# Optimization experiments

Hardware: AMD Instinct MI355X
Metric: run time of the kernel (lower is better)

The kernel has to match this reference:

```python
import jax, jax.numpy as jnp
import numpy as np

N_NODES = 100000
N_EDGES = 3200000
IN_CH = 256
OUT_CH = 256


def setup_inputs() -> dict:
    key = jax.random.key(0)
    k1, k2, k3, k4, k5 = jax.random.split(key, 5)
    x = jax.random.normal(k1, (N_NODES, IN_CH), dtype=jnp.float32)
    src = jax.random.randint(k2, (N_EDGES,), 0, N_NODES, dtype=jnp.int64)
    dst = jax.random.randint(k3, (N_EDGES,), 0, N_NODES, dtype=jnp.int64)
    # match torch uniform(in_channels, tensor): U(-1/sqrt(in), 1/sqrt(in))
    bound = 1.0 / np.sqrt(IN_CH)
    weight = jax.random.uniform(k4, (IN_CH, OUT_CH), minval=-bound, maxval=bound, dtype=jnp.float32)
    bias = jax.random.uniform(k5, (OUT_CH,), minval=-bound, maxval=bound, dtype=jnp.float32)
    return {"x": x, "src": src, "dst": dst, "weight": weight, "bias": bias}


def reference(x, src, dst, weight, bias):
    # paramApply: linear transform
    h = jnp.matmul(x, weight) + bias  # [N, out]
    # SpMM: out[dst] += h[src]  (unweighted adjacency, adj @ h)
    agg = jax.ops.segment_sum(h[src], dst, num_segments=N_NODES)  # [N, out]
    # row-degree normalization: adj.sum(-1) clamped at 1
    deg = jax.ops.segment_sum(jnp.ones((src.shape[0],), dtype=h.dtype), dst, num_segments=N_NODES)
    deg = jnp.maximum(deg, 1.0)[:, None]  # [N, 1]
    return agg / deg
```

## Files before the change

### kernel.cpp

```cpp
#include <hip/hip_runtime.h>

#define N_NODES 100000
#define N_EDGES 3200000
#define CH 256

#define NBUCK 256
#define NBUCK_USED 196
#define PBE 4096
#define EPT 16
#define PGRID ((N_EDGES + PBE - 1) / PBE)

#define WS_DEG    0
#define WS_OFF    524288
#define WS_BCNT   1048576
#define WS_BBASE  1049600
#define WS_BCUR   1050624
#define WS_WTB    1056768
#define WS_ESRC   1310720
#define WS_PACKED 14110720
#define WS_XB     14110720
#define WS_NEED_BF16X (WS_XB + (size_t)N_NODES * CH * 2)

typedef __bf16  bf16x8 __attribute__((ext_vector_type(8)));
typedef float   f32x4  __attribute__((ext_vector_type(4)));

__device__ __forceinline__ unsigned short f2bf(float f) {
    union { float f; unsigned u; } c; c.f = f;
    unsigned r = c.u + 0x7FFF + ((c.u >> 16) & 1);
    return (unsigned short)(r >> 16);
}
__device__ __forceinline__ float bf2f(unsigned short b) {
    union { unsigned u; float f; } c; c.u = (unsigned)b << 16;
    return c.f;
}

__global__ __launch_bounds__(256) void hist_k(const int* __restrict__ dst,
                                              int* __restrict__ bucket_cnt) {
    __shared__ int h[NBUCK];
    int t = threadIdx.x;
    h[t] = 0;
    __syncthreads();
    long e0 = (long)blockIdx.x * PBE;
#pragma unroll
    for (int i = 0; i < EPT; ++i) {
        long e = e0 + i * 256 + t;
        if (e < N_EDGES) atomicAdd(&h[dst[e] >> 9], 1);
    }
    __syncthreads();
    if (h[t]) atomicAdd(&bucket_cnt[t], h[t]);
}

__global__ void bscan_k(const int* __restrict__ cnt, int* __restrict__ base,
                        int* __restrict__ cursor) {
    __shared__ int s[NBUCK];
    int t = threadIdx.x;
    int v0 = cnt[t];
    s[t] = v0;
    __syncthreads();
    for (int st = 1; st < 256; st <<= 1) {
        int v = (t >= st) ? s[t - st] : 0;
        __syncthreads();
        s[t] += v;
        __syncthreads();
    }
    int excl = s[t] - v0;
    base[t] = excl;
    cursor[t] = excl;
}

__global__ __launch_bounds__(256) void partition_k(const int* __restrict__ src,
                                                   const int* __restrict__ dst,
                                                   int* __restrict__ bucket_cursor,
                                                   unsigned* __restrict__ packed) {
    __shared__ int hist[NBUCK];
    __shared__ int gbase[NBUCK];
    int t = threadIdx.x;
    hist[t] = 0;
    __syncthreads();
    long e0 = (long)blockIdx.x * PBE;
    int b[EPT], rank[EPT];
    unsigned pk[EPT];
#pragma unroll
    for (int i = 0; i < EPT; ++i) {
        long e = e0 + i * 256 + t;
        if (e < N_EDGES) {
            int d = dst[e];
            int s = src[e];
            b[i] = d >> 9;
            pk[i] = ((unsigned)(d & 511) << 17) | (unsigned)s;
            rank[i] = atomicAdd(&hist[b[i]], 1);
        } else b[i] = -1;
    }
    __syncthreads();
    int cnt = hist[t];
    if (cnt > 0) gbase[t] = atomicAdd(&bucket_cursor[t], cnt);
    __syncthreads();
#pragma unroll
    for (int i = 0; i < EPT; ++i)
        if (b[i] >= 0) packed[gbase[b[i]] + rank[i]] = pk[i];
}

__global__ __launch_bounds__(256) void build_k(const unsigned* __restrict__ packed,
                                               const int* __restrict__ bucket_base,
                                               const int* __restrict__ bucket_cnt,
                                               int* __restrict__ deg, int* __restrict__ off,
                                               int* __restrict__ edge_src) {
    __shared__ int ldeg[512];
    __shared__ int loff[512];
    __shared__ int lcur[512];
    __shared__ int sscan[256];
    int bk = blockIdx.x;
    int t = threadIdx.x;
    ldeg[t] = 0; ldeg[t + 256] = 0;
    __syncthreads();
    int ebase = bucket_base[bk];
    int ecnt  = bucket_cnt[bk];
    const unsigned* pk = packed + ebase;
    for (int i = t; i < ecnt; i += 256) atomicAdd(&ldeg[pk[i] >> 17], 1);
    __syncthreads();
    int a0 = ldeg[2 * t], a1 = ldeg[2 * t + 1];
    sscan[t] = a0 + a1;
    __syncthreads();
    for (int st = 1; st < 256; st <<= 1) {
        int v = (t >= st) ? sscan[t - st] : 0;
        __syncthreads();
        sscan[t] += v;
        __syncthreads();
    }
    int ex = sscan[t] - (a0 + a1);
    loff[2 * t] = ex;      lcur[2 * t] = ex;
    loff[2 * t + 1] = ex + a0;  lcur[2 * t + 1] = ex + a0;
    __syncthreads();
    int n0 = bk * 512;
#pragma unroll
    for (int j = 0; j < 2; ++j) {
        int dlow = t + j * 256;
        int node = n0 + dlow;
        if (node < N_NODES) {
            deg[node] = ldeg[dlow];
            off[node] = ebase + loff[dlow];
        }
    }
    int* es = edge_src + ebase;
    for (int i = t; i < ecnt; i += 256) {
        unsigned p = pk[i];
        int pos = atomicAdd(&lcur[p >> 17], 1);
        es[pos] = (int)(p & 0x1FFFF);
    }
}

__global__ void cast_w_k(const float* __restrict__ W, unsigned short* __restrict__ Wtb) {
    int n = blockIdx.x;
    int k = threadIdx.x;
    Wtb[n * 256 + k] = f2bf(W[k * 256 + n]);
}

__global__ void cast_x_k(const float* __restrict__ x, unsigned short* __restrict__ xb) {
    int i = blockIdx.x * 256 + threadIdx.x;
    float4 v = reinterpret_cast<const float4*>(x)[i];
    ushort4 o;
    o.x = f2bf(v.x); o.y = f2bf(v.y); o.z = f2bf(v.z); o.w = f2bf(v.w);
    reinterpret_cast<ushort4*>(xb)[i] = o;
}

__global__ void aggregate_bf16_k(const unsigned short* __restrict__ xb,
                                 const int* __restrict__ edge_src,
                                 const int* __restrict__ off, const int* __restrict__ deg,
                                 float* __restrict__ m) {
    int wid = threadIdx.x >> 6;
    int lane = threadIdx.x & 63;
    int node = blockIdx.x * 4 + wid;
    int start = off[node];
    int d = deg[node];
    float4 acc[4];
#pragma unroll
    for (int i = 0; i < 4; ++i) acc[i] = make_float4(0.f, 0.f, 0.f, 0.f);
    const unsigned short* xbl = xb + lane * 4;
    int e = 0;
    for (; e + 4 <= d; e += 4) {
        int s[4];
#pragma unroll
        for (int i = 0; i < 4; ++i) s[i] = edge_src[start + e + i];
#pragma unroll
        for (int i = 0; i < 4; ++i) {
            ushort4 v = *reinterpret_cast<const ushort4*>(xbl + (size_t)s[i] * CH);
            acc[i].x += bf2f(v.x); acc[i].y += bf2f(v.y);
            acc[i].z += bf2f(v.z); acc[i].w += bf2f(v.w);
        }
    }
    for (; e < d; ++e) {
        int s0 = edge_src[start + e];
        ushort4 v = *reinterpret_cast<const ushort4*>(xbl + (size_t)s0 * CH);
        acc[0].x += bf2f(v.x); acc[0].y += bf2f(v.y);
        acc[0].z += bf2f(v.z); acc[0].w += bf2f(v.w);
    }
    acc[0].x += acc[1].x + acc[2].x + acc[3].x;
    acc[0].y += acc[1].y + acc[2].y + acc[3].y;
    acc[0].z += acc[1].z + acc[2].z + acc[3].z;
    acc[0].w += acc[1].w + acc[2].w + acc[3].w;
    float inv = 1.0f / (float)(d > 0 ? d : 1);
    acc[0].x *= inv; acc[0].y *= inv; acc[0].z *= inv; acc[0].w *= inv;
    *reinterpret_cast<float4*>(m + (size_t)node * CH + lane * 4) = acc[0];
}

__global__ void aggregate_f32_k(const float* __restrict__ x, const int* __restrict__ edge_src,
                                const int* __restrict__ off, const int* __restrict__ deg,
                                float* __restrict__ m) {
    int wid = threadIdx.x >> 6;
    int lane = threadIdx.x & 63;
    int node = blockIdx.x * 4 + wid;
    int start = off[node];
    int d = deg[node];
    float4 acc0 = make_float4(0.f, 0.f, 0.f, 0.f);
    float4 acc1 = make_float4(0.f, 0.f, 0.f, 0.f);
    const float* xb = x + (size_t)lane * 4;
    int e = 0;
    for (; e + 2 <= d; e += 2) {
        int s0 = edge_src[start + e];
        int s1 = edge_src[start + e + 1];
        const float4 v0 = *reinterpret_cast<const float4*>(xb + (size_t)s0 * CH);
        const float4 v1 = *reinterpret_cast<const float4*>(xb + (size_t)s1 * CH);
        acc0.x += v0.x; acc0.y += v0.y; acc0.z += v0.z; acc0.w += v0.w;
        acc1.x += v1.x; acc1.y += v1.y; acc1.z += v1.z; acc1.w += v1.w;
    }
    if (e < d) {
        int s0 = edge_src[start + e];
        const float4 v0 = *reinterpret_cast<const float4*>(xb + (size_t)s0 * CH);
        acc0.x += v0.x; acc0.y += v0.y; acc0.z += v0.z; acc0.w += v0.w;
    }
    acc0.x += acc1.x; acc0.y += acc1.y; acc0.z += acc1.z; acc0.w += acc1.w;
    float inv = 1.0f / (float)(d > 0 ? d : 1);
    acc0.x *= inv; acc0.y *= inv; acc0.z *= inv; acc0.w *= inv;
    *reinterpret_cast<float4*>(m + (size_t)node * CH + lane * 4) = acc0;
}

__global__ __launch_bounds__(256) void gemm_mfma_k(float* __restrict__ io,
                                                   const unsigned short* __restrict__ Wtb,
                                                   const float* __restrict__ bias,
                                                   const int* __restrict__ deg) {
    __shared__ unsigned short As[64][264];
    int row0 = blockIdx.x * 64;
    int rows = N_NODES - row0;
    if (rows > 64) rows = 64;
    int tid = threadIdx.x;

#pragma unroll
    for (int i = 0; i < 16; ++i) {
        int f = i * 256 + tid;
        int r = f >> 6;
        int c4 = (f & 63) * 4;
        float4 v = make_float4(0.f, 0.f, 0.f, 0.f);
        if (r < rows)
            v = *reinterpret_cast<const float4*>(io + (size_t)(row0 + r) * CH + c4);
        ushort4 o;
        o.x = f2bf(v.x); o.y = f2bf(v.y); o.z = f2bf(v.z); o.w = f2bf(v.w);
        *reinterpret_cast<ushort4*>(&As[r][c4]) = o;
    }
    __syncthreads();

    int wv = tid >> 6;
    int lane = tid & 63;
    int q = lane >> 4;
    int ln = lane & 15;
    int n0 = wv * 64;

    f32x4 acc[4][4];
#pragma unroll
    for (int mt = 0; mt < 4; ++mt)
#pragma unroll
        for (int nt = 0; nt < 4; ++nt)
            acc[mt][nt] = (f32x4){0.f, 0.f, 0.f, 0.f};

#pragma unroll 2
    for (int kc = 0; kc < 8; ++kc) {
        int koff = kc * 32 + q * 8;
        bf16x8 a[4], b[4];
#pragma unroll
        for (int mt = 0; mt < 4; ++mt)
            a[mt] = *reinterpret_cast<const bf16x8*>(&As[mt * 16 + ln][koff]);
#pragma unroll
        for (int nt = 0; nt < 4; ++nt)
            b[nt] = *reinterpret_cast<const bf16x8*>(Wtb + (size_t)(n0 + nt * 16 + ln) * 256 + koff);
#pragma unroll
        for (int mt = 0; mt < 4; ++mt)
#pragma unroll
            for (int nt = 0; nt < 4; ++nt)
                acc[mt][nt] = __builtin_amdgcn_mfma_f32_16x16x32_bf16(a[mt], b[nt], acc[mt][nt], 0, 0, 0);
    }

    float bv[4];
#pragma unroll
    for (int nt = 0; nt < 4; ++nt) bv[nt] = bias[n0 + nt * 16 + ln];

#pragma unroll
    for (int mt = 0; mt < 4; ++mt) {
#pragma unroll
        for (int r = 0; r < 4; ++r) {
            int row = row0 + mt * 16 + q * 4 + r;
            if (row < N_NODES) {
                float bon = (deg[row] > 0) ? 1.f : 0.f;
                float* po = io + (size_t)row * CH + n0 + ln;
#pragma unroll
                for (int nt = 0; nt < 4; ++nt)
                    po[nt * 16] = acc[mt][nt][r] + bv[nt] * bon;
            }
        }
    }
}

extern "C" void kernel_launch(void* const* d_in, const int* in_sizes, int n_in,
                              void* d_out, int out_size, void* d_ws, size_t ws_size,
                              hipStream_t stream) {
    const float* x    = (const float*)d_in[0];
    const int*   src  = (const int*)d_in[1];
    const int*   dst  = (const int*)d_in[2];
    const float* W    = (const float*)d_in[3];
    const float* bias = (const float*)d_in[4];
    float* out = (float*)d_out;

    char* ws = (char*)d_ws;
    int* deg        = (int*)(ws + WS_DEG);
    int* off        = (int*)(ws + WS_OFF);
    int* bcnt       = (int*)(ws + WS_BCNT);
    int* bbase      = (int*)(ws + WS_BBASE);
    int* bcur       = (int*)(ws + WS_BCUR);
    unsigned short* Wtb = (unsigned short*)(ws + WS_WTB);
    int* edge_src   = (int*)(ws + WS_ESRC);
    unsigned* packed = (unsigned*)(ws + WS_PACKED);
    unsigned short* xb = (unsigned short*)(ws + WS_XB);

    bool use_bf16x = ws_size >= WS_NEED_BF16X;

    hipMemsetAsync(bcnt, 0, NBUCK * sizeof(int), stream);

    hist_k<<<PGRID, 256, 0, stream>>>(dst, bcnt);
    bscan_k<<<1, 256, 0, stream>>>(bcnt, bbase, bcur);
    partition_k<<<PGRID, 256, 0, stream>>>(src, dst, bcur, packed);
    build_k<<<NBUCK_USED, 256, 0, stream>>>(packed, bbase, bcnt, deg, off, edge_src);

    cast_w_k<<<256, 256, 0, stream>>>(W, Wtb);

    if (use_bf16x) {
        cast_x_k<<<(N_NODES * CH / 4) / 256, 256, 0, stream>>>(x, xb);
        aggregate_bf16_k<<<N_NODES / 4, 256, 0, stream>>>(xb, edge_src, off, deg, out);
    } else {
        aggregate_f32_k<<<N_NODES / 4, 256, 0, stream>>>(x, edge_src, off, deg, out);
    }

    gemm_mfma_k<<<(N_NODES + 63) / 64, 256, 0, stream>>>(out, Wtb, bias, deg);
}
```

Baseline: 568.6 us.

## Apply linear transform before aggregation and gather bf16 transformed features

Reorders the computation so the MFMA GEMM runs on x first, producing bias-added h stored as bf16, then aggregates h over edges and normalizes into the output. This removes the separate x cast pass and the GEMM's read-modify-write of the full f32 output, cutting global memory traffic. The aggregation loop is also unrolled to 8 gathers in flight and uses readfirstlane for offsets and degree. Rounding h (rather than x) to bf16 slightly changes numerical error characteristics.

```diff
diff --git a/kernel.cpp b/kernel.cpp
--- a/kernel.cpp
+++ b/kernel.cpp
@@ -18,8 +18,8 @@
 #define WS_WTB    1056768
 #define WS_ESRC   1310720
 #define WS_PACKED 14110720
-#define WS_XB     14110720
-#define WS_NEED_BF16X (WS_XB + (size_t)N_NODES * CH * 2)
+#define WS_HB     14110720
+#define WS_NEED_H (WS_HB + (size_t)N_NODES * CH * 2)
 
 typedef __bf16  bf16x8 __attribute__((ext_vector_type(8)));
 typedef float   f32x4  __attribute__((ext_vector_type(4)));
@@ -155,42 +155,122 @@
     Wtb[n * 256 + k] = f2bf(W[k * 256 + n]);
 }
 
-__global__ void cast_x_k(const float* __restrict__ x, unsigned short* __restrict__ xb) {
-    int i = blockIdx.x * 256 + threadIdx.x;
-    float4 v = reinterpret_cast<const float4*>(x)[i];
-    ushort4 o;
-    o.x = f2bf(v.x); o.y = f2bf(v.y); o.z = f2bf(v.z); o.w = f2bf(v.w);
-    reinterpret_cast<ushort4*>(xb)[i] = o;
-}
-
-__global__ void aggregate_bf16_k(const unsigned short* __restrict__ xb,
-                                 const int* __restrict__ edge_src,
-                                 const int* __restrict__ off, const int* __restrict__ deg,
-                                 float* __restrict__ m) {
+__global__ __launch_bounds__(256) void gemm_h_k(const float* __restrict__ x,
+                                                const unsigned short* __restrict__ Wtb,
+                                                const float* __restrict__ bias,
+                                                unsigned short* __restrict__ hb) {
+    __shared__ unsigned short As[64][264];
+    int row0 = blockIdx.x * 64;
+    int rows = N_NODES - row0;
+    if (rows > 64) rows = 64;
+    int tid = threadIdx.x;
+
+#pragma unroll
+    for (int i = 0; i < 16; ++i) {
+        int f = i * 256 + tid;
+        int r = f >> 6;
+        int c4 = (f & 63) * 4;
+        float4 v = make_float4(0.f, 0.f, 0.f, 0.f);
+        if (r < rows)
+            v = *reinterpret_cast<const float4*>(x + (size_t)(row0 + r) * CH + c4);
+        ushort4 o;
+        o.x = f2bf(v.x); o.y = f2bf(v.y); o.z = f2bf(v.z); o.w = f2bf(v.w);
+        *reinterpret_cast<ushort4*>(&As[r][c4]) = o;
+    }
+    __syncthreads();
+
+    int wv = tid >> 6;
+    int lane = tid & 63;
+    int q = lane >> 4;
+    int ln = lane & 15;
+    int n0 = wv * 64;
+
+    f32x4 acc[4][4];
+#pragma unroll
+    for (int mt = 0; mt < 4; ++mt)
+#pragma unroll
+        for (int nt = 0; nt < 4; ++nt)
+            acc[mt][nt] = (f32x4){0.f, 0.f, 0.f, 0.f};
+
+#pragma unroll 2
+    for (int kc = 0; kc < 8; ++kc) {
+        int koff = kc * 32 + q * 8;
+        bf16x8 a[4], b[4];
+#pragma unroll
+        for (int mt = 0; mt < 4; ++mt)
+            a[mt] = *reinterpret_cast<const bf16x8*>(&As[mt * 16 + ln][koff]);
+#pragma unroll
+        for (int nt = 0; nt < 4; ++nt)
+            b[nt] = *reinterpret_cast<const bf16x8*>(Wtb + (size_t)(n0 + nt * 16 + ln) * 256 + koff);
+#pragma unroll
+        for (int mt = 0; mt < 4; ++mt)
+#pragma unroll
+            for (int nt = 0; nt < 4; ++nt)
+                acc[mt][nt] = __builtin_amdgcn_mfma_f32_16x16x32_bf16(a[mt], b[nt], acc[mt][nt], 0, 0, 0);
+    }
+
+    float bv[4];
+#pragma unroll
+    for (int nt = 0; nt < 4; ++nt) bv[nt] = bias[n0 + nt * 16 + ln];
+
+#pragma unroll
+    for (int mt = 0; mt < 4; ++mt) {
+#pragma unroll
+        for (int r = 0; r < 4; ++r) {
+            int row = row0 + mt * 16 + q * 4 + r;
+            if (row < N_NODES) {
+                unsigned short* po = hb + (size_t)row * CH + n0 + ln;
+#pragma unroll
+                for (int nt = 0; nt < 4; ++nt)
+                    po[nt * 16] = f2bf(acc[mt][nt][r] + bv[nt]);
+            }
+        }
+    }
+}
+
+__global__ void aggregate_h_k(const unsigned short* __restrict__ hb,
+                              const int* __restrict__ edge_src,
+                              const int* __restrict__ off, const int* __restrict__ deg,
+                              float* __restrict__ out) {
     int wid = threadIdx.x >> 6;
     int lane = threadIdx.x & 63;
     int node = blockIdx.x * 4 + wid;
-    int start = off[node];
-    int d = deg[node];
+    int start = __builtin_amdgcn_readfirstlane(off[node]);
+    int d     = __builtin_amdgcn_readfirstlane(deg[node]);
     float4 acc[4];
 #pragma unroll
     for (int i = 0; i < 4; ++i) acc[i] = make_float4(0.f, 0.f, 0.f, 0.f);
-    const unsigned short* xbl = xb + lane * 4;
+    const unsigned short* hbl = hb + lane * 4;
+    const int* es = edge_src + start;
     int e = 0;
+    for (; e + 8 <= d; e += 8) {
+        int s[8];
+#pragma unroll
+        for (int i = 0; i < 8; ++i) s[i] = es[e + i];
+        ushort4 v[8];
+#pragma unroll
+        for (int i = 0; i < 8; ++i)
+            v[i] = *reinterpret_cast<const ushort4*>(hbl + (size_t)s[i] * CH);
+#pragma unroll
+        for (int i = 0; i < 8; ++i) {
+            acc[i & 3].x += bf2f(v[i].x); acc[i & 3].y += bf2f(v[i].y);
+            acc[i & 3].z += bf2f(v[i].z); acc[i & 3].w += bf2f(v[i].w);
+        }
+    }
     for (; e + 4 <= d; e += 4) {
         int s[4];
 #pragma unroll
-        for (int i = 0; i < 4; ++i) s[i] = edge_src[start + e + i];
+        for (int i = 0; i < 4; ++i) s[i] = es[e + i];
 #pragma unroll
         for (int i = 0; i < 4; ++i) {
-            ushort4 v = *reinterpret_cast<const ushort4*>(xbl + (size_t)s[i] * CH);
+            ushort4 v = *reinterpret_cast<const ushort4*>(hbl + (size_t)s[i] * CH);
             acc[i].x += bf2f(v.x); acc[i].y += bf2f(v.y);
             acc[i].z += bf2f(v.z); acc[i].w += bf2f(v.w);
         }
     }
     for (; e < d; ++e) {
-        int s0 = edge_src[start + e];
-        ushort4 v = *reinterpret_cast<const ushort4*>(xbl + (size_t)s0 * CH);
+        int s0 = es[e];
+        ushort4 v = *reinterpret_cast<const ushort4*>(hbl + (size_t)s0 * CH);
         acc[0].x += bf2f(v.x); acc[0].y += bf2f(v.y);
         acc[0].z += bf2f(v.z); acc[0].w += bf2f(v.w);
     }
@@ -200,7 +280,7 @@
     acc[0].w += acc[1].w + acc[2].w + acc[3].w;
     float inv = 1.0f / (float)(d > 0 ? d : 1);
     acc[0].x *= inv; acc[0].y *= inv; acc[0].z *= inv; acc[0].w *= inv;
-    *reinterpret_cast<float4*>(m + (size_t)node * CH + lane * 4) = acc[0];
+    *reinterpret_cast<float4*>(out + (size_t)node * CH + lane * 4) = acc[0];
 }
 
 __global__ void aggregate_f32_k(const float* __restrict__ x, const int* __restrict__ edge_src,
@@ -243,7 +323,6 @@
     int rows = N_NODES - row0;
     if (rows > 64) rows = 64;
     int tid = threadIdx.x;
-
 #pragma unroll
     for (int i = 0; i < 16; ++i) {
         int f = i * 256 + tid;
@@ -257,20 +336,17 @@
         *reinterpret_cast<ushort4*>(&As[r][c4]) = o;
     }
     __syncthreads();
-
     int wv = tid >> 6;
     int lane = tid & 63;
     int q = lane >> 4;
     int ln = lane & 15;
     int n0 = wv * 64;
-
     f32x4 acc[4][4];
 #pragma unroll
     for (int mt = 0; mt < 4; ++mt)
 #pragma unroll
         for (int nt = 0; nt < 4; ++nt)
             acc[mt][nt] = (f32x4){0.f, 0.f, 0.f, 0.f};
-
 #pragma unroll 2
     for (int kc = 0; kc < 8; ++kc) {
         int koff = kc * 32 + q * 8;
@@ -287,11 +363,9 @@
             for (int nt = 0; nt < 4; ++nt)
                 acc[mt][nt] = __builtin_amdgcn_mfma_f32_16x16x32_bf16(a[mt], b[nt], acc[mt][nt], 0, 0, 0);
     }
-
     float bv[4];
 #pragma unroll
     for (int nt = 0; nt < 4; ++nt) bv[nt] = bias[n0 + nt * 16 + ln];
-
 #pragma unroll
     for (int mt = 0; mt < 4; ++mt) {
 #pragma unroll
@@ -327,9 +401,9 @@
     unsigned short* Wtb = (unsigned short*)(ws + WS_WTB);
     int* edge_src   = (int*)(ws + WS_ESRC);
     unsigned* packed = (unsigned*)(ws + WS_PACKED);
-    unsigned short* xb = (unsigned short*)(ws + WS_XB);
-
-    bool use_bf16x = ws_size >= WS_NEED_BF16X;
+    unsigned short* hb = (unsigned short*)(ws + WS_HB);
+
+    bool use_h = ws_size >= WS_NEED_H;
 
     hipMemsetAsync(bcnt, 0, NBUCK * sizeof(int), stream);
 
@@ -340,12 +414,11 @@
 
     cast_w_k<<<256, 256, 0, stream>>>(W, Wtb);
 
-    if (use_bf16x) {
-        cast_x_k<<<(N_NODES * CH / 4) / 256, 256, 0, stream>>>(x, xb);
-        aggregate_bf16_k<<<N_NODES / 4, 256, 0, stream>>>(xb, edge_src, off, deg, out);
+    if (use_h) {
+        gemm_h_k<<<(N_NODES + 63) / 64, 256, 0, stream>>>(x, Wtb, bias, hb);
+        aggregate_h_k<<<N_NODES / 4, 256, 0, stream>>>(hb, edge_src, off, deg, out);
     } else {
         aggregate_f32_k<<<N_NODES / 4, 256, 0, stream>>>(x, edge_src, off, deg, out);
-    }
-
-    gemm_mfma_k<<<(N_NODES + 63) / 64, 256, 0, stream>>>(out, Wtb, bias, deg);
-}
+        gemm_mfma_k<<<(N_NODES + 63) / 64, 256, 0, stream>>>(out, Wtb, bias, deg);
+    }
+}
```

Measured after the change: 560.8 us. About the same (-1.4%).
